# Performance work log

Measured on AMD Instinct MI355X. Metric: run time of the kernel, lower is better.

Reference implementation:

```python
import jax, jax.numpy as jnp
import numpy as np

B, L, D = 8, 2048, 1024   # batch, seq_len, d_model
E, H, K = 8, 512, 2       # num_experts, expert_hidden, top_k
LN_EPS = 1e-5


def setup_inputs() -> dict:
    key = jax.random.key(0)
    ks = jax.random.split(key, 4)
    rn = lambda k, shape, sc: (jax.random.normal(k, shape, jnp.float32) * sc)
    return {
        "x": rn(ks[0], (B, L, D), 1.0),
        "ln_w": jnp.ones((D,), jnp.float32),
        "ln_b": jnp.zeros((D,), jnp.float32),
        "gate_w": rn(ks[1], (D, E), 0.02),
        "gate_b": jnp.zeros((E,), jnp.float32),
        "w1": rn(ks[2], (E, D, H), 0.02),
        "b1": jnp.zeros((E, H), jnp.float32),
        "w2": rn(ks[3], (E, H, D), 0.02),
        "b2": jnp.zeros((E, D), jnp.float32),
    }


def reference(x, ln_w, ln_b, gate_w, gate_b, w1, b1, w2, b2):
    Bx, Lx, Dx = x.shape
    xf = x.reshape(-1, Dx)                                   # [N, D]

    # gate = LayerNorm -> Linear (eval mode: no noise)
    mu = xf.mean(-1, keepdims=True)
    var = ((xf - mu) ** 2).mean(-1, keepdims=True)
    xn = (xf - mu) * jax.lax.rsqrt(var + LN_EPS) * ln_w + ln_b
    gate_logits = xn @ gate_w + gate_b                       # [N, E]
    gate_weights = jax.nn.softmax(gate_logits, axis=-1)      # [N, E]

    top_w, top_idx = jax.lax.top_k(gate_weights, K)          # [N, K]
    top_w = top_w / top_w.sum(-1, keepdims=True)

    # dense all-experts compute (faithful to the torch module)
    h = jax.nn.gelu(jnp.einsum('nd,edh->neh', xf, w1) + b1, approximate=False)  # [N, E, H]
    expert_out = jnp.einsum('neh,ehd->ned', h, w2) + b2      # [N, E, D]

    # gather selected experts and weighted-combine
    sel = jnp.take_along_axis(expert_out, top_idx[:, :, None], axis=1)  # [N, K, D]
    out = (top_w[:, :, None] * sel).sum(axis=1).reshape(Bx, Lx, Dx)
    return out, gate_weights
```

## Files before the change

kernel.cpp:

```cpp
#include <hip/hip_runtime.h>
#include <hip/hip_bf16.h>

#define N_TOK 16384
#define DM 1024
#define HD 512
#define NE 8
#define LN_EPS 1e-5f
#define MT_MAX 264

typedef __attribute__((ext_vector_type(8))) short v8s;
typedef __attribute__((ext_vector_type(4))) float v4f;

typedef const __attribute__((address_space(1))) unsigned int* as1cu;
typedef __attribute__((address_space(3))) unsigned int* as3u;

__device__ __forceinline__ void gl_lds16(const void* g, void* l) {
  __builtin_amdgcn_global_load_lds((as1cu)g, (as3u)l, 16, 0, 0);
}

__device__ __forceinline__ unsigned short f2bf(float f) {
  union { float f; unsigned u; } c; c.f = f;
  unsigned u = c.u + 0x7FFFu + ((c.u >> 16) & 1u);
  return (unsigned short)(u >> 16);
}

__device__ __forceinline__ float bf2f(unsigned short v) {
  union { unsigned u; float f; } c; c.u = ((unsigned)v) << 16;
  return c.f;
}

__device__ __forceinline__ float gelu_f(float v) {
  return 0.5f * v * (1.0f + erff(v * 0.7071067811865475f));
}

__global__ __launch_bounds__(256) void gate_kernel(
    const float* __restrict__ x, const float* __restrict__ lnw,
    const float* __restrict__ lnb, const float* __restrict__ gw,
    const float* __restrict__ gb, float* __restrict__ gates_out,
    int* __restrict__ ce, float* __restrict__ cw,
    unsigned short* __restrict__ xbf)
{
  const int wv = threadIdx.x >> 6, l = threadIdx.x & 63;
  const int n = blockIdx.x * 4 + wv;
  const float* xr = x + (size_t)n * DM;
  float4 v[4]; float s = 0.f, s2 = 0.f;
#pragma unroll
  for (int j = 0; j < 4; ++j) {
    v[j] = *(const float4*)(xr + l * 4 + j * 256);
    s  += v[j].x + v[j].y + v[j].z + v[j].w;
    s2 += v[j].x * v[j].x + v[j].y * v[j].y + v[j].z * v[j].z + v[j].w * v[j].w;
  }
  {
    unsigned long long* xbo = (unsigned long long*)(xbf + (size_t)n * DM);
#pragma unroll
    for (int j = 0; j < 4; ++j) {
      union { unsigned short u[4]; unsigned long long ll; } pk;
      pk.u[0] = f2bf(v[j].x); pk.u[1] = f2bf(v[j].y);
      pk.u[2] = f2bf(v[j].z); pk.u[3] = f2bf(v[j].w);
      xbo[l + j * 64] = pk.ll;
    }
  }
#pragma unroll
  for (int m = 1; m < 64; m <<= 1) { s += __shfl_xor(s, m); s2 += __shfl_xor(s2, m); }
  const float mu = s * (1.f / DM);
  const float var = s2 * (1.f / DM) - mu * mu;
  const float rstd = 1.f / sqrtf(var + LN_EPS);
  float acc[8] = {0, 0, 0, 0, 0, 0, 0, 0};
#pragma unroll
  for (int j = 0; j < 4; ++j) {
#pragma unroll
    for (int q = 0; q < 4; ++q) {
      int d = l * 4 + j * 256 + q;
      float xv = (q == 0) ? v[j].x : (q == 1) ? v[j].y : (q == 2) ? v[j].z : v[j].w;
      float xn = (xv - mu) * rstd * lnw[d] + lnb[d];
      const float4 g0 = *(const float4*)(gw + d * 8);
      const float4 g1 = *(const float4*)(gw + d * 8 + 4);
      acc[0] += xn * g0.x; acc[1] += xn * g0.y; acc[2] += xn * g0.z; acc[3] += xn * g0.w;
      acc[4] += xn * g1.x; acc[5] += xn * g1.y; acc[6] += xn * g1.z; acc[7] += xn * g1.w;
    }
  }
#pragma unroll
  for (int e = 0; e < 8; ++e)
#pragma unroll
    for (int m = 1; m < 64; m <<= 1) acc[e] += __shfl_xor(acc[e], m);

  if (l == 0) {
    float lg[8], p[8], g[8];
    float mx = -1e30f;
    for (int e = 0; e < 8; ++e) { lg[e] = acc[e] + gb[e]; mx = fmaxf(mx, lg[e]); }
    float sum = 0.f;
    for (int e = 0; e < 8; ++e) { p[e] = expf(lg[e] - mx); sum += p[e]; }
    float inv = 1.f / sum;
    for (int e = 0; e < 8; ++e) g[e] = p[e] * inv;
    float4* go = (float4*)(gates_out + (size_t)n * 8);
    go[0] = make_float4(g[0], g[1], g[2], g[3]);
    go[1] = make_float4(g[4], g[5], g[6], g[7]);
    int e0 = 0; float b0 = g[0];
    for (int e = 1; e < 8; ++e) if (g[e] > b0) { b0 = g[e]; e0 = e; }
    int e1 = -1; float b1v = -1.f;
    for (int e = 0; e < 8; ++e) if (e != e0 && g[e] > b1v) { b1v = g[e]; e1 = e; }
    float wsum = b0 + b1v;
    ce[2 * n] = e0; ce[2 * n + 1] = e1;
    cw[2 * n] = b0 / wsum; cw[2 * n + 1] = b1v / wsum;
  }
}

__global__ __launch_bounds__(256) void route_kernel(
    const int* __restrict__ ce, const float* __restrict__ cw,
    int* __restrict__ counts, int* __restrict__ tids, float* __restrict__ pws)
{
  __shared__ int cnt;
  const int e = blockIdx.x;
  if (threadIdx.x == 0) cnt = 0;
  __syncthreads();
  for (int i = threadIdx.x; i < 2 * N_TOK; i += 256) {
    if (ce[i] == e) {
      int p = atomicAdd(&cnt, 1);
      tids[e * N_TOK + p] = i;
      pws[e * N_TOK + p] = cw[i];
    }
  }
  __syncthreads();
  if (threadIdx.x == 0) counts[e] = cnt;
}

__global__ __launch_bounds__(256) void transpose_cvt(
    const float* __restrict__ in, unsigned short* __restrict__ out, int R, int C)
{
  __shared__ float tile[64][65];
  const int tilesC = C >> 6, tilesR = R >> 6;
  const int perE = tilesR * tilesC;
  int bt = blockIdx.x;
  const int e = bt / perE; int rem = bt - e * perE;
  const int tr = rem / tilesC, tc = rem - tr * tilesC;
  const float* ip = in + (size_t)e * R * C;
  unsigned short* op = out + (size_t)e * R * C;
  const int r0 = tr * 64, c0 = tc * 64;
#pragma unroll
  for (int i = 0; i < 16; ++i) {
    int idx = i * 256 + threadIdx.x;
    int rr = idx >> 6, cc = idx & 63;
    tile[rr][cc] = ip[(size_t)(r0 + rr) * C + (c0 + cc)];
  }
  __syncthreads();
#pragma unroll
  for (int i = 0; i < 16; ++i) {
    int idx = i * 256 + threadIdx.x;
    int rr = idx >> 6, cc = idx & 63;
    op[(size_t)(c0 + rr) * R + (r0 + cc)] = f2bf(tile[cc][rr]);
  }
}

__global__ __launch_bounds__(256) void gemm1w_kernel(
    const unsigned short* __restrict__ xbf, const unsigned short* __restrict__ w1t,
    const float* __restrict__ b1,
    const int* __restrict__ counts, const int* __restrict__ tids,
    unsigned short* __restrict__ hbuf)
{
  __shared__ unsigned short As[128 * 64];
  __shared__ unsigned short Bs[256 * 64];
  __shared__ int tokL[128];
  __shared__ int sE, sBase, sCnt;

  const int t = threadIdx.x;
  const int bid = blockIdx.x;
  const int nt = bid / MT_MAX;
  const int mt = bid - nt * MT_MAX;

  if (t == 0) {
    int pref = 0, e = -1, base = 0, cn = 0;
    for (int i = 0; i < NE; ++i) {
      int c = counts[i];
      int tiles = (c + 127) >> 7;
      if (mt < pref + tiles) { e = i; base = (mt - pref) << 7; cn = c; break; }
      pref += tiles;
    }
    sE = e; sBase = base; sCnt = cn;
  }
  __syncthreads();
  const int e = sE;
  if (e < 0) return;
  const int cnt = sCnt, baseI = sBase;

  if (t < 128) {
    int i = baseI + t;
    tokL[t] = ((i < cnt) ? tids[e * N_TOK + i] : tids[e * N_TOK]) >> 1;
  }
  __syncthreads();

  const unsigned short* gA[4];
#pragma unroll
  for (int i = 0; i < 4; ++i) {
    int c = i * 256 + t;
    int row = c >> 3, ks = c & 7;
    gA[i] = xbf + (size_t)tokL[row] * DM + (ks ^ (row & 7)) * 8;
  }
  const unsigned short* gB0;
  {
    int row = t >> 3, ks = t & 7;
    gB0 = w1t + ((size_t)e * HD + nt * 256 + row) * DM + (ks ^ (row & 7)) * 8;
  }
  const int w = t >> 6, l = t & 63;
  const int wr = w >> 1, wc = w & 1;
  const int lrow = l & 15, lhi = l >> 4;
  char* AsB = (char*)As;
  char* BsB = (char*)Bs;
  char* ldsA = AsB + w * 1024;
  char* ldsB = BsB + w * 1024;

  v4f acc[4][8];
#pragma unroll
  for (int a = 0; a < 4; ++a)
#pragma unroll
    for (int b = 0; b < 8; ++b) acc[a][b] = (v4f){0.f, 0.f, 0.f, 0.f};

  for (int kt = 0; kt < 16; ++kt) {
    __syncthreads();
#pragma unroll
    for (int i = 0; i < 4; ++i)
      gl_lds16(gA[i] + kt * 64, ldsA + i * 4096);
#pragma unroll
    for (int i = 0; i < 8; ++i)
      gl_lds16(gB0 + (size_t)i * 32 * DM + kt * 64, ldsB + i * 4096);
    __syncthreads();
#pragma unroll
    for (int ks2 = 0; ks2 < 2; ++ks2) {
      const int sb = ks2 * 4 + lhi;
      v8s a[4], b[8];
#pragma unroll
      for (int mi = 0; mi < 4; ++mi) {
        int row = wr * 64 + mi * 16 + lrow;
        a[mi] = *(const v8s*)(AsB + row * 128 + ((sb ^ (row & 7)) << 4));
      }
#pragma unroll
      for (int nj = 0; nj < 8; ++nj) {
        int col = wc * 128 + nj * 16 + lrow;
        b[nj] = *(const v8s*)(BsB + col * 128 + ((sb ^ (col & 7)) << 4));
      }
#pragma unroll
      for (int mi = 0; mi < 4; ++mi)
#pragma unroll
        for (int nj = 0; nj < 8; ++nj)
          acc[mi][nj] = __builtin_amdgcn_mfma_f32_16x16x32_bf16(a[mi], b[nj], acc[mi][nj], 0, 0, 0);
    }
  }

#pragma unroll
  for (int nj = 0; nj < 8; ++nj) {
    const int col = nt * 256 + wc * 128 + nj * 16 + lrow;
    const float bb = b1[e * HD + col];
#pragma unroll
    for (int mi = 0; mi < 4; ++mi) {
      const int row0 = wr * 64 + mi * 16 + lhi * 4;
#pragma unroll
      for (int r = 0; r < 4; ++r) {
        float g = gelu_f(acc[mi][nj][r] + bb);
        hbuf[(size_t)(mt * 128 + row0 + r) * HD + col] = f2bf(g);
      }
    }
  }
}

__global__ __launch_bounds__(256) void gemm2w_kernel(
    const unsigned short* __restrict__ hbuf, const unsigned short* __restrict__ w2t,
    const float* __restrict__ b2,
    const int* __restrict__ counts, const int* __restrict__ tids,
    const float* __restrict__ pws, unsigned short* __restrict__ obuf)
{
  __shared__ unsigned short As[128 * 64];
  __shared__ unsigned short Bs[256 * 64];
  __shared__ int pidL[128];
  __shared__ float wtL[128];
  __shared__ int sE, sBase, sCnt;

  const int t = threadIdx.x;
  const int bid = blockIdx.x;
  const int nt = bid / MT_MAX;
  const int mt = bid - nt * MT_MAX;

  if (t == 0) {
    int pref = 0, e = -1, base = 0, cn = 0;
    for (int i = 0; i < NE; ++i) {
      int c = counts[i];
      int tiles = (c + 127) >> 7;
      if (mt < pref + tiles) { e = i; base = (mt - pref) << 7; cn = c; break; }
      pref += tiles;
    }
    sE = e; sBase = base; sCnt = cn;
  }
  __syncthreads();
  const int e = sE;
  if (e < 0) return;
  const int cnt = sCnt, baseI = sBase;

  if (t < 128) {
    int i = baseI + t;
    bool ok = i < cnt;
    pidL[t] = ok ? tids[e * N_TOK + i] : 0;
    wtL[t] = ok ? pws[e * N_TOK + i] : 0.f;
  }
  __syncthreads();

  const unsigned short* gA0;
  const unsigned short* gB0;
  {
    int row = t >> 3, ks = t & 7;
    int kswz = (ks ^ (row & 7)) * 8;
    gA0 = hbuf + (size_t)(mt * 128 + row) * HD + kswz;
    gB0 = w2t + ((size_t)e * DM + nt * 256 + row) * HD + kswz;
  }
  const int w = t >> 6, l = t & 63;
  const int wr = w >> 1, wc = w & 1;
  const int lrow = l & 15, lhi = l >> 4;
  char* AsB = (char*)As;
  char* BsB = (char*)Bs;
  char* ldsA = AsB + w * 1024;
  char* ldsB = BsB + w * 1024;

  v4f acc[4][8];
#pragma unroll
  for (int a = 0; a < 4; ++a)
#pragma unroll
    for (int b = 0; b < 8; ++b) acc[a][b] = (v4f){0.f, 0.f, 0.f, 0.f};

  for (int kt = 0; kt < 8; ++kt) {
    __syncthreads();
#pragma unroll
    for (int i = 0; i < 4; ++i)
      gl_lds16(gA0 + (size_t)i * 32 * HD + kt * 64, ldsA + i * 4096);
#pragma unroll
    for (int i = 0; i < 8; ++i)
      gl_lds16(gB0 + (size_t)i * 32 * HD + kt * 64, ldsB + i * 4096);
    __syncthreads();
#pragma unroll
    for (int ks2 = 0; ks2 < 2; ++ks2) {
      const int sb = ks2 * 4 + lhi;
      v8s a[4], b[8];
#pragma unroll
      for (int mi = 0; mi < 4; ++mi) {
        int row = wr * 64 + mi * 16 + lrow;
        a[mi] = *(const v8s*)(AsB + row * 128 + ((sb ^ (row & 7)) << 4));
      }
#pragma unroll
      for (int nj = 0; nj < 8; ++nj) {
        int col = wc * 128 + nj * 16 + lrow;
        b[nj] = *(const v8s*)(BsB + col * 128 + ((sb ^ (col & 7)) << 4));
      }
#pragma unroll
      for (int mi = 0; mi < 4; ++mi)
#pragma unroll
        for (int nj = 0; nj < 8; ++nj)
          acc[mi][nj] = __builtin_amdgcn_mfma_f32_16x16x32_bf16(a[mi], b[nj], acc[mi][nj], 0, 0, 0);
    }
  }

#pragma unroll
  for (int nj = 0; nj < 8; ++nj) {
    const int col = nt * 256 + wc * 128 + nj * 16 + lrow;
    const float bb = b2[e * DM + col];
#pragma unroll
    for (int mi = 0; mi < 4; ++mi) {
      const int rbase = wr * 64 + mi * 16 + lhi * 4;
#pragma unroll
      for (int r = 0; r < 4; ++r) {
        const int rloc = rbase + r;
        if (baseI + rloc < cnt) {
          float val = wtL[rloc] * (acc[mi][nj][r] + bb);
          obuf[(size_t)pidL[rloc] * DM + col] = f2bf(val);
        }
      }
    }
  }
}

__global__ __launch_bounds__(256) void combine_kernel(
    const unsigned short* __restrict__ obuf, float* __restrict__ outp)
{
  const int CH = N_TOK * (DM / 8);
  for (int i = blockIdx.x * 256 + threadIdx.x; i < CH; i += gridDim.x * 256) {
    const int n = i >> 7, rem = i & 127;
    const v8s a = *(const v8s*)(obuf + ((size_t)(2 * n)) * DM + rem * 8);
    const v8s b = *(const v8s*)(obuf + ((size_t)(2 * n + 1)) * DM + rem * 8);
    float o[8];
#pragma unroll
    for (int j = 0; j < 8; ++j)
      o[j] = bf2f((unsigned short)a[j]) + bf2f((unsigned short)b[j]);
    float* dst = outp + (size_t)n * DM + rem * 8;
    *(float4*)dst = make_float4(o[0], o[1], o[2], o[3]);
    *(float4*)(dst + 4) = make_float4(o[4], o[5], o[6], o[7]);
  }
}

__global__ __launch_bounds__(256, 3) void gemm2_kernel(
    const unsigned short* __restrict__ hbuf, const unsigned short* __restrict__ w2t,
    const float* __restrict__ b2,
    const int* __restrict__ counts, const int* __restrict__ tids,
    const float* __restrict__ pws, float* __restrict__ outp)
{
  __shared__ unsigned short As[128 * 64];
  __shared__ unsigned short Bs[128 * 64];
  __shared__ int tokL[128];
  __shared__ float wtL[128];
  __shared__ int sE, sBase, sCnt;

  const int t = threadIdx.x;
  const int bid = blockIdx.x;
  const int nt = bid / MT_MAX;
  const int mt = bid - nt * MT_MAX;

  if (t == 0) {
    int pref = 0, e = -1, base = 0, cn = 0;
    for (int i = 0; i < NE; ++i) {
      int c = counts[i];
      int tiles = (c + 127) >> 7;
      if (mt < pref + tiles) { e = i; base = (mt - pref) << 7; cn = c; break; }
      pref += tiles;
    }
    sE = e; sBase = base; sCnt = cn;
  }
  __syncthreads();
  const int e = sE;
  if (e < 0) return;
  const int cnt = sCnt, baseI = sBase;

  if (t < 128) {
    int i = baseI + t;
    bool ok = i < cnt;
    tokL[t] = ok ? (tids[e * N_TOK + i] >> 1) : 0;
    wtL[t] = ok ? pws[e * N_TOK + i] : 0.f;
  }
  __syncthreads();

  const unsigned short* gA[4];
  const unsigned short* gB[4];
#pragma unroll
  for (int i = 0; i < 4; ++i) {
    int c = i * 256 + t;
    int row = c >> 3, ks = c & 7;
    int kswz = ks ^ (row & 7);
    gA[i] = hbuf + (size_t)(mt * 128 + row) * HD + kswz * 8;
    gB[i] = w2t + ((size_t)e * DM + nt * 128 + row) * HD + kswz * 8;
  }
  const int w = t >> 6, l = t & 63;
  const int wr = w >> 1, wc = w & 1;
  const int lrow = l & 15, lhi = l >> 4;
  char* AsB = (char*)As;
  char* BsB = (char*)Bs;
  char* ldsA = AsB + w * 1024;
  char* ldsB = BsB + w * 1024;

  v4f acc[4][4];
#pragma unroll
  for (int a = 0; a < 4; ++a)
#pragma unroll
    for (int b = 0; b < 4; ++b) acc[a][b] = (v4f){0.f, 0.f, 0.f, 0.f};

  for (int kt = 0; kt < 8; ++kt) {
    __syncthreads();
#pragma unroll
    for (int i = 0; i < 4; ++i) {
      gl_lds16(gA[i] + kt * 64, ldsA + i * 4096);
      gl_lds16(gB[i] + kt * 64, ldsB + i * 4096);
    }
    __syncthreads();
#pragma unroll
    for (int ks2 = 0; ks2 < 2; ++ks2) {
      const int sb = ks2 * 4 + lhi;
      v8s a[4], b[4];
#pragma unroll
      for (int mi = 0; mi < 4; ++mi) {
        int row = wr * 64 + mi * 16 + lrow;
        a[mi] = *(const v8s*)(AsB + row * 128 + ((sb ^ (row & 7)) << 4));
      }
#pragma unroll
      for (int nj = 0; nj < 4; ++nj) {
        int col = wc * 64 + nj * 16 + lrow;
        b[nj] = *(const v8s*)(BsB + col * 128 + ((sb ^ (col & 7)) << 4));
      }
#pragma unroll
      for (int mi = 0; mi < 4; ++mi)
#pragma unroll
        for (int nj = 0; nj < 4; ++nj)
          acc[mi][nj] = __builtin_amdgcn_mfma_f32_16x16x32_bf16(a[mi], b[nj], acc[mi][nj], 0, 0, 0);
    }
  }

#pragma unroll
  for (int nj = 0; nj < 4; ++nj) {
    const int col = nt * 128 + wc * 64 + nj * 16 + lrow;
    const float bb = b2[e * DM + col];
#pragma unroll
    for (int mi = 0; mi < 4; ++mi) {
      const int rbase = wr * 64 + mi * 16 + lhi * 4;
#pragma unroll
      for (int r = 0; r < 4; ++r) {
        const int rloc = rbase + r;
        if (baseI + rloc < cnt) {
          float val = wtL[rloc] * (acc[mi][nj][r] + bb);
          atomicAdd(outp + (size_t)tokL[rloc] * DM + col, val);
        }
      }
    }
  }
}

extern "C" void kernel_launch(void* const* d_in, const int* in_sizes, int n_in,
                              void* d_out, int out_size, void* d_ws, size_t ws_size,
                              hipStream_t stream)
{
  const float* x   = (const float*)d_in[0];
  const float* lnw = (const float*)d_in[1];
  const float* lnb = (const float*)d_in[2];
  const float* gw  = (const float*)d_in[3];
  const float* gb  = (const float*)d_in[4];
  const float* w1  = (const float*)d_in[5];
  const float* b1  = (const float*)d_in[6];
  const float* w2  = (const float*)d_in[7];
  const float* b2  = (const float*)d_in[8];
  float* out = (float*)d_out;
  float* gates_out = out + (size_t)N_TOK * DM;

  char* ws = (char*)d_ws;
  int*   ce     = (int*)(ws + 0);
  float* cw     = (float*)(ws + 131072);
  int*   counts = (int*)(ws + 262144);
  int*   tids   = (int*)(ws + 262400);
  float* pws    = (float*)(ws + 786688);
  unsigned short* w1t  = (unsigned short*)(ws + 1310976);
  unsigned short* w2t  = (unsigned short*)(ws + 9699584);
  unsigned short* xbf  = (unsigned short*)(ws + 18088192);
  unsigned short* hbuf = (unsigned short*)(ws + 51642624);
  unsigned short* obuf = (unsigned short*)(ws + 86245632);
  const size_t NEED_V3 = 153354496ull;

  gate_kernel<<<N_TOK / 4, 256, 0, stream>>>(x, lnw, lnb, gw, gb, gates_out, ce, cw, xbf);
  route_kernel<<<NE, 256, 0, stream>>>(ce, cw, counts, tids, pws);
  transpose_cvt<<<NE * 16 * 8, 256, 0, stream>>>(w1, w1t, DM, HD);
  transpose_cvt<<<NE * 8 * 16, 256, 0, stream>>>(w2, w2t, HD, DM);
  gemm1w_kernel<<<2 * MT_MAX, 256, 0, stream>>>(xbf, w1t, b1, counts, tids, hbuf);

  if (ws_size >= NEED_V3) {
    gemm2w_kernel<<<4 * MT_MAX, 256, 0, stream>>>(hbuf, w2t, b2, counts, tids, pws, obuf);
    combine_kernel<<<2048, 256, 0, stream>>>(obuf, out);
  } else {
    hipMemsetAsync(out, 0, (size_t)N_TOK * DM * sizeof(float), stream);
    gemm2_kernel<<<8 * MT_MAX, 256, 0, stream>>>(hbuf, w2t, b2, counts, tids, pws, out);
  }
}
```

Baseline: 595.7 us.

## Prefetch next K tile in expert GEMMs, shrink tiles, write obuf in slot order

Both grouped expert GEMMs now use 128x128 tiles instead of 128x256, with launch_bounds(256,4) for higher occupancy. The K loop copies fragments from LDS into registers, then issues the global-to-LDS loads for the next K tile before running the MFMAs, so loads overlap compute. GEMM2 writes results contiguously in sorted-slot order rather than scattering rows by pair id. A new slot_kernel builds a pair-to-slot map, and the combine kernel gathers through it. This adds one small launch and an indirect gather, and reuses the ce workspace region for the slot map.

Measured after the change: 732.1 us. 1.23x slower.

```diff
diff --git a/kernel.cpp b/kernel.cpp
--- a/kernel.cpp
+++ b/kernel.cpp
@@ -124,6 +124,19 @@
   if (threadIdx.x == 0) counts[e] = cnt;
 }
 
+__global__ __launch_bounds__(256) void slot_kernel(
+    const int* __restrict__ counts, const int* __restrict__ tids,
+    int* __restrict__ sl)
+{
+  const int e = blockIdx.x;
+  int tb = 0;
+  for (int i = 0; i < e; ++i) tb += ((counts[i] + 127) >> 7);
+  tb <<= 7;
+  const int cnt = counts[e];
+  for (int pos = threadIdx.x; pos < cnt; pos += 256)
+    sl[tids[e * N_TOK + pos]] = tb + pos;
+}
+
 __global__ __launch_bounds__(256) void transpose_cvt(
     const float* __restrict__ in, unsigned short* __restrict__ out, int R, int C)
 {
@@ -151,14 +164,14 @@
   }
 }
 
-__global__ __launch_bounds__(256) void gemm1w_kernel(
+__global__ __launch_bounds__(256, 4) void gemm1p_kernel(
     const unsigned short* __restrict__ xbf, const unsigned short* __restrict__ w1t,
     const float* __restrict__ b1,
     const int* __restrict__ counts, const int* __restrict__ tids,
     unsigned short* __restrict__ hbuf)
 {
   __shared__ unsigned short As[128 * 64];
-  __shared__ unsigned short Bs[256 * 64];
+  __shared__ unsigned short Bs[128 * 64];
   __shared__ int tokL[128];
   __shared__ int sE, sBase, sCnt;
 
@@ -189,16 +202,14 @@
   __syncthreads();
 
   const unsigned short* gA[4];
+  const unsigned short* gB[4];
 #pragma unroll
   for (int i = 0; i < 4; ++i) {
     int c = i * 256 + t;
     int row = c >> 3, ks = c & 7;
-    gA[i] = xbf + (size_t)tokL[row] * DM + (ks ^ (row & 7)) * 8;
-  }
-  const unsigned short* gB0;
-  {
-    int row = t >> 3, ks = t & 7;
-    gB0 = w1t + ((size_t)e * HD + nt * 256 + row) * DM + (ks ^ (row & 7)) * 8;
+    int kswz = (ks ^ (row & 7)) * 8;
+    gA[i] = xbf + (size_t)tokL[row] * DM + kswz;
+    gB[i] = w1t + ((size_t)e * HD + nt * 128 + row) * DM + kswz;
   }
   const int w = t >> 6, l = t & 63;
   const int wr = w >> 1, wc = w & 1;
@@ -208,46 +219,57 @@
   char* ldsA = AsB + w * 1024;
   char* ldsB = BsB + w * 1024;
 
-  v4f acc[4][8];
+  v4f acc[4][4];
 #pragma unroll
   for (int a = 0; a < 4; ++a)
 #pragma unroll
-    for (int b = 0; b < 8; ++b) acc[a][b] = (v4f){0.f, 0.f, 0.f, 0.f};
+    for (int b = 0; b < 4; ++b) acc[a][b] = (v4f){0.f, 0.f, 0.f, 0.f};
+
+#pragma unroll
+  for (int i = 0; i < 4; ++i) {
+    gl_lds16(gA[i], ldsA + i * 4096);
+    gl_lds16(gB[i], ldsB + i * 4096);
+  }
 
   for (int kt = 0; kt < 16; ++kt) {
     __syncthreads();
-#pragma unroll
-    for (int i = 0; i < 4; ++i)
-      gl_lds16(gA[i] + kt * 64, ldsA + i * 4096);
-#pragma unroll
-    for (int i = 0; i < 8; ++i)
-      gl_lds16(gB0 + (size_t)i * 32 * DM + kt * 64, ldsB + i * 4096);
+    v8s a0[4], a1[4], b0[4], b1[4];
+#pragma unroll
+    for (int mi = 0; mi < 4; ++mi) {
+      int row = wr * 64 + mi * 16 + lrow;
+      a0[mi] = *(const v8s*)(AsB + row * 128 + (((lhi)     ^ (row & 7)) << 4));
+      a1[mi] = *(const v8s*)(AsB + row * 128 + (((4 + lhi) ^ (row & 7)) << 4));
+    }
+#pragma unroll
+    for (int nj = 0; nj < 4; ++nj) {
+      int col = wc * 64 + nj * 16 + lrow;
+      b0[nj] = *(const v8s*)(BsB + col * 128 + (((lhi)     ^ (col & 7)) << 4));
+      b1[nj] = *(const v8s*)(BsB + col * 128 + (((4 + lhi) ^ (col & 7)) << 4));
+    }
     __syncthreads();
-#pragma unroll
-    for (int ks2 = 0; ks2 < 2; ++ks2) {
-      const int sb = ks2 * 4 + lhi;
-      v8s a[4], b[8];
-#pragma unroll
-      for (int mi = 0; mi < 4; ++mi) {
-        int row = wr * 64 + mi * 16 + lrow;
-        a[mi] = *(const v8s*)(AsB + row * 128 + ((sb ^ (row & 7)) << 4));
-      }
-#pragma unroll
-      for (int nj = 0; nj < 8; ++nj) {
-        int col = wc * 128 + nj * 16 + lrow;
-        b[nj] = *(const v8s*)(BsB + col * 128 + ((sb ^ (col & 7)) << 4));
-      }
-#pragma unroll
-      for (int mi = 0; mi < 4; ++mi)
-#pragma unroll
-        for (int nj = 0; nj < 8; ++nj)
-          acc[mi][nj] = __builtin_amdgcn_mfma_f32_16x16x32_bf16(a[mi], b[nj], acc[mi][nj], 0, 0, 0);
-    }
-  }
-
-#pragma unroll
-  for (int nj = 0; nj < 8; ++nj) {
-    const int col = nt * 256 + wc * 128 + nj * 16 + lrow;
+    if (kt < 15) {
+#pragma unroll
+      for (int i = 0; i < 4; ++i) {
+        gl_lds16(gA[i] + (kt + 1) * 64, ldsA + i * 4096);
+        gl_lds16(gB[i] + (kt + 1) * 64, ldsB + i * 4096);
+      }
+    }
+    __builtin_amdgcn_sched_barrier(0);
+#pragma unroll
+    for (int mi = 0; mi < 4; ++mi)
+#pragma unroll
+      for (int nj = 0; nj < 4; ++nj)
+        acc[mi][nj] = __builtin_amdgcn_mfma_f32_16x16x32_bf16(a0[mi], b0[nj], acc[mi][nj], 0, 0, 0);
+#pragma unroll
+    for (int mi = 0; mi < 4; ++mi)
+#pragma unroll
+      for (int nj = 0; nj < 4; ++nj)
+        acc[mi][nj] = __builtin_amdgcn_mfma_f32_16x16x32_bf16(a1[mi], b1[nj], acc[mi][nj], 0, 0, 0);
+  }
+
+#pragma unroll
+  for (int nj = 0; nj < 4; ++nj) {
+    const int col = nt * 128 + wc * 64 + nj * 16 + lrow;
     const float bb = b1[e * HD + col];
 #pragma unroll
     for (int mi = 0; mi < 4; ++mi) {
@@ -261,15 +283,14 @@
   }
 }
 
-__global__ __launch_bounds__(256) void gemm2w_kernel(
+__global__ __launch_bounds__(256, 4) void gemm2p_kernel(
     const unsigned short* __restrict__ hbuf, const unsigned short* __restrict__ w2t,
     const float* __restrict__ b2,
     const int* __restrict__ counts, const int* __restrict__ tids,
     const float* __restrict__ pws, unsigned short* __restrict__ obuf)
 {
   __shared__ unsigned short As[128 * 64];
-  __shared__ unsigned short Bs[256 * 64];
-  __shared__ int pidL[128];
+  __shared__ unsigned short Bs[128 * 64];
   __shared__ float wtL[128];
   __shared__ int sE, sBase, sCnt;
 
@@ -295,19 +316,19 @@
 
   if (t < 128) {
     int i = baseI + t;
-    bool ok = i < cnt;
-    pidL[t] = ok ? tids[e * N_TOK + i] : 0;
-    wtL[t] = ok ? pws[e * N_TOK + i] : 0.f;
-  }
-  __syncthreads();
-
-  const unsigned short* gA0;
-  const unsigned short* gB0;
-  {
-    int row = t >> 3, ks = t & 7;
+    wtL[t] = (i < cnt) ? pws[e * N_TOK + i] : 0.f;
+  }
+  __syncthreads();
+
+  const unsigned short* gA[4];
+  const unsigned short* gB[4];
+#pragma unroll
+  for (int i = 0; i < 4; ++i) {
+    int c = i * 256 + t;
+    int row = c >> 3, ks = c & 7;
     int kswz = (ks ^ (row & 7)) * 8;
-    gA0 = hbuf + (size_t)(mt * 128 + row) * HD + kswz;
-    gB0 = w2t + ((size_t)e * DM + nt * 256 + row) * HD + kswz;
+    gA[i] = hbuf + (size_t)(mt * 128 + row) * HD + kswz;
+    gB[i] = w2t + ((size_t)e * DM + nt * 128 + row) * HD + kswz;
   }
   const int w = t >> 6, l = t & 63;
   const int wr = w >> 1, wc = w & 1;
@@ -317,46 +338,57 @@
   char* ldsA = AsB + w * 1024;
   char* ldsB = BsB + w * 1024;
 
-  v4f acc[4][8];
+  v4f acc[4][4];
 #pragma unroll
   for (int a = 0; a < 4; ++a)
 #pragma unroll
-    for (int b = 0; b < 8; ++b) acc[a][b] = (v4f){0.f, 0.f, 0.f, 0.f};
+    for (int b = 0; b < 4; ++b) acc[a][b] = (v4f){0.f, 0.f, 0.f, 0.f};
+
+#pragma unroll
+  for (int i = 0; i < 4; ++i) {
+    gl_lds16(gA[i], ldsA + i * 4096);
+    gl_lds16(gB[i], ldsB + i * 4096);
+  }
 
   for (int kt = 0; kt < 8; ++kt) {
     __syncthreads();
-#pragma unroll
-    for (int i = 0; i < 4; ++i)
-      gl_lds16(gA0 + (size_t)i * 32 * HD + kt * 64, ldsA + i * 4096);
-#pragma unroll
-    for (int i = 0; i < 8; ++i)
-      gl_lds16(gB0 + (size_t)i * 32 * HD + kt * 64, ldsB + i * 4096);
+    v8s a0[4], a1[4], b0[4], b1[4];
+#pragma unroll
+    for (int mi = 0; mi < 4; ++mi) {
+      int row = wr * 64 + mi * 16 + lrow;
+      a0[mi] = *(const v8s*)(AsB + row * 128 + (((lhi)     ^ (row & 7)) << 4));
+      a1[mi] = *(const v8s*)(AsB + row * 128 + (((4 + lhi) ^ (row & 7)) << 4));
+    }
+#pragma unroll
+    for (int nj = 0; nj < 4; ++nj) {
+      int col = wc * 64 + nj * 16 + lrow;
+      b0[nj] = *(const v8s*)(BsB + col * 128 + (((lhi)     ^ (col & 7)) << 4));
+      b1[nj] = *(const v8s*)(BsB + col * 128 + (((4 + lhi) ^ (col & 7)) << 4));
+    }
     __syncthreads();
-#pragma unroll
-    for (int ks2 = 0; ks2 < 2; ++ks2) {
-      const int sb = ks2 * 4 + lhi;
-      v8s a[4], b[8];
-#pragma unroll
-      for (int mi = 0; mi < 4; ++mi) {
-        int row = wr * 64 + mi * 16 + lrow;
-        a[mi] = *(const v8s*)(AsB + row * 128 + ((sb ^ (row & 7)) << 4));
-      }
-#pragma unroll
-      for (int nj = 0; nj < 8; ++nj) {
-        int col = wc * 128 + nj * 16 + lrow;
-        b[nj] = *(const v8s*)(BsB + col * 128 + ((sb ^ (col & 7)) << 4));
-      }
-#pragma unroll
-      for (int mi = 0; mi < 4; ++mi)
-#pragma unroll
-        for (int nj = 0; nj < 8; ++nj)
-          acc[mi][nj] = __builtin_amdgcn_mfma_f32_16x16x32_bf16(a[mi], b[nj], acc[mi][nj], 0, 0, 0);
-    }
-  }
-
-#pragma unroll
-  for (int nj = 0; nj < 8; ++nj) {
-    const int col = nt * 256 + wc * 128 + nj * 16 + lrow;
+    if (kt < 7) {
+#pragma unroll
+      for (int i = 0; i < 4; ++i) {
+        gl_lds16(gA[i] + (kt + 1) * 64, ldsA + i * 4096);
+        gl_lds16(gB[i] + (kt + 1) * 64, ldsB + i * 4096);
+      }
+    }
+    __builtin_amdgcn_sched_barrier(0);
+#pragma unroll
+    for (int mi = 0; mi < 4; ++mi)
+#pragma unroll
+      for (int nj = 0; nj < 4; ++nj)
+        acc[mi][nj] = __builtin_amdgcn_mfma_f32_16x16x32_bf16(a0[mi], b0[nj], acc[mi][nj], 0, 0, 0);
+#pragma unroll
+    for (int mi = 0; mi < 4; ++mi)
+#pragma unroll
+      for (int nj = 0; nj < 4; ++nj)
+        acc[mi][nj] = __builtin_amdgcn_mfma_f32_16x16x32_bf16(a1[mi], b1[nj], acc[mi][nj], 0, 0, 0);
+  }
+
+#pragma unroll
+  for (int nj = 0; nj < 4; ++nj) {
+    const int col = nt * 128 + wc * 64 + nj * 16 + lrow;
     const float bb = b2[e * DM + col];
 #pragma unroll
     for (int mi = 0; mi < 4; ++mi) {
@@ -364,23 +396,23 @@
 #pragma unroll
       for (int r = 0; r < 4; ++r) {
         const int rloc = rbase + r;
-        if (baseI + rloc < cnt) {
-          float val = wtL[rloc] * (acc[mi][nj][r] + bb);
-          obuf[(size_t)pidL[rloc] * DM + col] = f2bf(val);
-        }
+        float val = wtL[rloc] * (acc[mi][nj][r] + bb);
+        obuf[(size_t)(mt * 128 + rloc) * DM + col] = f2bf(val);
       }
     }
   }
 }
 
 __global__ __launch_bounds__(256) void combine_kernel(
-    const unsigned short* __restrict__ obuf, float* __restrict__ outp)
+    const unsigned short* __restrict__ obuf, const int* __restrict__ sl,
+    float* __restrict__ outp)
 {
   const int CH = N_TOK * (DM / 8);
   for (int i = blockIdx.x * 256 + threadIdx.x; i < CH; i += gridDim.x * 256) {
     const int n = i >> 7, rem = i & 127;
-    const v8s a = *(const v8s*)(obuf + ((size_t)(2 * n)) * DM + rem * 8);
-    const v8s b = *(const v8s*)(obuf + ((size_t)(2 * n + 1)) * DM + rem * 8);
+    const int s0 = sl[2 * n], s1 = sl[2 * n + 1];
+    const v8s a = *(const v8s*)(obuf + (size_t)s0 * DM + rem * 8);
+    const v8s b = *(const v8s*)(obuf + (size_t)s1 * DM + rem * 8);
     float o[8];
 #pragma unroll
     for (int j = 0; j < 8; ++j)
@@ -531,17 +563,19 @@
   unsigned short* xbf  = (unsigned short*)(ws + 18088192);
   unsigned short* hbuf = (unsigned short*)(ws + 51642624);
   unsigned short* obuf = (unsigned short*)(ws + 86245632);
-  const size_t NEED_V3 = 153354496ull;
+  int* sl = (int*)(ws + 0);
+  const size_t NEED_V4 = 86245632ull + (size_t)MT_MAX * 128 * DM * 2;
 
   gate_kernel<<<N_TOK / 4, 256, 0, stream>>>(x, lnw, lnb, gw, gb, gates_out, ce, cw, xbf);
   route_kernel<<<NE, 256, 0, stream>>>(ce, cw, counts, tids, pws);
   transpose_cvt<<<NE * 16 * 8, 256, 0, stream>>>(w1, w1t, DM, HD);
   transpose_cvt<<<NE * 8 * 16, 256, 0, stream>>>(w2, w2t, HD, DM);
-  gemm1w_kernel<<<2 * MT_MAX, 256, 0, stream>>>(xbf, w1t, b1, counts, tids, hbuf);
-
-  if (ws_size >= NEED_V3) {
-    gemm2w_kernel<<<4 * MT_MAX, 256, 0, stream>>>(hbuf, w2t, b2, counts, tids, pws, obuf);
-    combine_kernel<<<2048, 256, 0, stream>>>(obuf, out);
+  gemm1p_kernel<<<4 * MT_MAX, 256, 0, stream>>>(xbf, w1t, b1, counts, tids, hbuf);
+
+  if (ws_size >= NEED_V4) {
+    slot_kernel<<<NE, 256, 0, stream>>>(counts, tids, sl);
+    gemm2p_kernel<<<8 * MT_MAX, 256, 0, stream>>>(hbuf, w2t, b2, counts, tids, pws, obuf);
+    combine_kernel<<<2048, 256, 0, stream>>>(obuf, sl, out);
   } else {
     hipMemsetAsync(out, 0, (size_t)N_TOK * DM * sizeof(float), stream);
     gemm2_kernel<<<8 * MT_MAX, 256, 0, stream>>>(hbuf, w2t, b2, counts, tids, pws, out);
```
